# Kernel tuning notes

Hardware: AMD Instinct MI355X
Metric: run time of the kernel (lower is better)

## Reference

```python
import jax, jax.numpy as jnp
import numpy as np

B, C, H, W = 64, 512, 64, 64
RED = 16
HID = C // RED  # 32
N_EXPERTS = 3

def setup_inputs() -> dict:
    key = jax.random.key(0)
    k1, k2, k3, k4 = jax.random.split(key, 4)
    x = jax.random.normal(k1, (B, C, H, W), dtype=jnp.float32)
    dataset = jax.random.randint(k2, (B,), 0, N_EXPERTS, dtype=jnp.int32)
    # torch Linear weight layout: [out_features, in_features]
    W1 = jax.random.normal(k3, (N_EXPERTS, HID, C), dtype=jnp.float32) * (1.0 / np.sqrt(C))
    W2 = jax.random.normal(k4, (N_EXPERTS, C, HID), dtype=jnp.float32) * (1.0 / np.sqrt(HID))
    return {"x": x, "dataset": dataset, "W1": W1, "W2": W2}

def reference(x, dataset, W1, W2):
    # global average pool: [B, C]
    y = jnp.mean(x, axis=(2, 3))
    # per-sample expert weights, routed by dataset id
    w1 = W1[dataset]  # [B, HID, C]
    w2 = W2[dataset]  # [B, C, HID]
    h = jax.nn.relu(jnp.einsum('bc,bhc->bh', y, w1))
    gate = jax.nn.sigmoid(jnp.einsum('bh,bch->bc', h, w2))  # [B, C]
    return x * gate[:, :, None, None]
```

## Files before the change

### kernel.cpp

```cpp
#include <hip/hip_runtime.h>
#include <math.h>

#define NB 64
#define NC 512
#define NHW 4096
#define NHID 32

__global__ __launch_bounds__(256) void pool_kernel(const float* __restrict__ x,
                                                   float* __restrict__ y) {
    const int bc = blockIdx.x;
    const float4* __restrict__ xin =
        reinterpret_cast<const float4*>(x + (size_t)bc * NHW);
    const int tid = threadIdx.x;

    float s = 0.f;
#pragma unroll
    for (int i = 0; i < 4; ++i) {
        float4 v = xin[tid + i * 256];
        s += v.x + v.y + v.z + v.w;
    }
#pragma unroll
    for (int o = 32; o; o >>= 1) s += __shfl_down(s, o, 64);

    __shared__ float partial[4];
    const int wid = tid >> 6;
    if ((tid & 63) == 0) partial[wid] = s;
    __syncthreads();
    if (tid == 0) {
        float t = partial[0] + partial[1] + partial[2] + partial[3];
        y[bc] = t * (1.0f / NHW);
    }
}

__global__ __launch_bounds__(256) void gate_kernel(const float* __restrict__ y,
                                                   const int* __restrict__ dataset,
                                                   const float* __restrict__ W1,
                                                   const float* __restrict__ W2,
                                                   float* __restrict__ gate) {
    const int b = blockIdx.x;
    const int tid = threadIdx.x;

    __shared__ float ys[NC];
    __shared__ float hs[NHID];

    ys[tid]       = y[b * NC + tid];
    ys[tid + 256] = y[b * NC + tid + 256];
    const int e = dataset[b];
    __syncthreads();

    const int hid = tid >> 3;
    const int j   = tid & 7;
    const float* __restrict__ w1row = W1 + ((size_t)e * NHID + hid) * NC;
    float acc = 0.f;
    for (int c = j; c < NC; c += 8) acc += ys[c] * w1row[c];
#pragma unroll
    for (int o = 4; o; o >>= 1) acc += __shfl_down(acc, o, 8);
    if (j == 0) hs[hid] = fmaxf(acc, 0.f);
    __syncthreads();

    const float* __restrict__ w2base = W2 + (size_t)e * NC * NHID;
#pragma unroll
    for (int k = 0; k < 2; ++k) {
        const int c = tid + k * 256;
        const float* __restrict__ w2row = w2base + c * NHID;
        float z = 0.f;
#pragma unroll
        for (int hh = 0; hh < NHID; ++hh) z += hs[hh] * w2row[hh];
        gate[b * NC + c] = 1.0f / (1.0f + expf(-z));
    }
}

__global__ __launch_bounds__(256) void scale_kernel(const float* __restrict__ x,
                                                    const float* __restrict__ gate,
                                                    float* __restrict__ out) {
    const size_t total4 = (size_t)NB * NC * NHW / 4;
    const size_t stride = (size_t)gridDim.x * blockDim.x;
    for (size_t i = (size_t)blockIdx.x * 256 + threadIdx.x; i < total4; i += stride) {
        const float g = gate[i >> 10];
        float4 v = reinterpret_cast<const float4*>(x)[i];
        v.x *= g; v.y *= g; v.z *= g; v.w *= g;
        reinterpret_cast<float4*>(out)[i] = v;
    }
}

extern "C" void kernel_launch(void* const* d_in, const int* in_sizes, int n_in,
                              void* d_out, int out_size, void* d_ws, size_t ws_size,
                              hipStream_t stream) {
    const float* x       = (const float*)d_in[0];
    const int*   dataset = (const int*)d_in[1];
    const float* W1      = (const float*)d_in[2];
    const float* W2      = (const float*)d_in[3];
    float* out = (float*)d_out;

    float* y    = (float*)d_ws;
    float* gate = y + NB * NC;

    pool_kernel<<<NB * NC, 256, 0, stream>>>(x, y);
    gate_kernel<<<NB, 256, 0, stream>>>(y, dataset, W1, W2, gate);
    scale_kernel<<<2048, 256, 0, stream>>>(x, gate, out);
}
```

Baseline: 353.4 us.

## Use wave-per-plane pooling and reverse-order scale with nontemporal stores

```diff
diff --git a/kernel.cpp b/kernel.cpp
--- a/kernel.cpp
+++ b/kernel.cpp
@@ -5,31 +5,27 @@
 #define NC 512
 #define NHW 4096
 #define NHID 32
+#define NPLANES (NB * NC)
+
+typedef float f32x4 __attribute__((ext_vector_type(4)));
 
 __global__ __launch_bounds__(256) void pool_kernel(const float* __restrict__ x,
                                                    float* __restrict__ y) {
-    const int bc = blockIdx.x;
-    const float4* __restrict__ xin =
-        reinterpret_cast<const float4*>(x + (size_t)bc * NHW);
-    const int tid = threadIdx.x;
+    const int wid   = threadIdx.x >> 6;
+    const int lane  = threadIdx.x & 63;
+    const int plane = blockIdx.x * 4 + wid;
+    const f32x4* __restrict__ xin =
+        reinterpret_cast<const f32x4*>(x + (size_t)plane * NHW);
 
     float s = 0.f;
 #pragma unroll
-    for (int i = 0; i < 4; ++i) {
-        float4 v = xin[tid + i * 256];
+    for (int i = 0; i < 16; ++i) {
+        f32x4 v = xin[lane + i * 64];
         s += v.x + v.y + v.z + v.w;
     }
 #pragma unroll
     for (int o = 32; o; o >>= 1) s += __shfl_down(s, o, 64);
-
-    __shared__ float partial[4];
-    const int wid = tid >> 6;
-    if ((tid & 63) == 0) partial[wid] = s;
-    __syncthreads();
-    if (tid == 0) {
-        float t = partial[0] + partial[1] + partial[2] + partial[3];
-        y[bc] = t * (1.0f / NHW);
-    }
+    if (lane == 0) y[plane] = s * (1.0f / NHW);
 }
 
 __global__ __launch_bounds__(256) void gate_kernel(const float* __restrict__ y,
@@ -73,13 +69,28 @@
 __global__ __launch_bounds__(256) void scale_kernel(const float* __restrict__ x,
                                                     const float* __restrict__ gate,
                                                     float* __restrict__ out) {
-    const size_t total4 = (size_t)NB * NC * NHW / 4;
-    const size_t stride = (size_t)gridDim.x * blockDim.x;
-    for (size_t i = (size_t)blockIdx.x * 256 + threadIdx.x; i < total4; i += stride) {
-        const float g = gate[i >> 10];
-        float4 v = reinterpret_cast<const float4*>(x)[i];
-        v.x *= g; v.y *= g; v.z *= g; v.w *= g;
-        reinterpret_cast<float4*>(out)[i] = v;
+    const int pair = (NPLANES / 2 - 1) - blockIdx.x;
+    const int p0 = pair * 2;
+    const float g0 = gate[p0];
+    const float g1 = gate[p0 + 1];
+    const size_t base = (size_t)pair * 2048;
+    const f32x4* __restrict__ xin = reinterpret_cast<const f32x4*>(x);
+    f32x4* __restrict__ o4 = reinterpret_cast<f32x4*>(out);
+    const int t = threadIdx.x;
+
+#pragma unroll
+    for (int k = 0; k < 4; ++k) {
+        const size_t i = base + (size_t)k * 256 + t;
+        f32x4 v = xin[i];
+        v *= g0;
+        __builtin_nontemporal_store(v, &o4[i]);
+    }
+#pragma unroll
+    for (int k = 0; k < 4; ++k) {
+        const size_t i = base + 1024 + (size_t)k * 256 + t;
+        f32x4 v = xin[i];
+        v *= g1;
+        __builtin_nontemporal_store(v, &o4[i]);
     }
 }
 
@@ -95,7 +106,7 @@
     float* y    = (float*)d_ws;
     float* gate = y + NB * NC;
 
-    pool_kernel<<<NB * NC, 256, 0, stream>>>(x, y);
+    pool_kernel<<<NPLANES / 4, 256, 0, stream>>>(x, y);
     gate_kernel<<<NB, 256, 0, stream>>>(y, dataset, W1, W2, gate);
-    scale_kernel<<<2048, 256, 0, stream>>>(x, gate, out);
+    scale_kernel<<<NPLANES / 2, 256, 0, stream>>>(x, gate, out);
 }
```

Result: faster. 284.9 us (-19.4%).

## Fuse pool, gate and scale into one persistent kernel holding x in registers

Applied to the files above, without the earlier changes.

```diff
diff --git a/kernel.cpp b/kernel.cpp
--- a/kernel.cpp
+++ b/kernel.cpp
@@ -5,81 +5,139 @@
 #define NC 512
 #define NHW 4096
 #define NHID 32
+#define GRID 512
+#define BLK 256
+#define DSLOT 6
+#define OWNER_LAG 3
+#define CONS_LAG 6
 
-__global__ __launch_bounds__(256) void pool_kernel(const float* __restrict__ x,
-                                                   float* __restrict__ y) {
-    const int bc = blockIdx.x;
-    const float4* __restrict__ xin =
-        reinterpret_cast<const float4*>(x + (size_t)bc * NHW);
-    const int tid = threadIdx.x;
+typedef float f32x4 __attribute__((ext_vector_type(4)));
 
-    float s = 0.f;
+
+__global__ __launch_bounds__(BLK, 2) void fused_kernel(
+        const float* __restrict__ x,
+        const int* __restrict__ dataset,
+        const float* __restrict__ W1,
+        const float* __restrict__ W2,
+        float* __restrict__ out,
+        unsigned* __restrict__ done1,
+        unsigned* __restrict__ gready,
+        float* __restrict__ y,
+        float* __restrict__ gate) {
+    const int tid  = threadIdx.x;
+    const int blk  = blockIdx.x;
+    const int wid  = tid >> 6;
+    const int lane = tid & 63;
+    const int c0   = blk;
+    const int grp  = blk >> 3;
+
+    __shared__ float part[4];
+    __shared__ float ysl[NC];
+    __shared__ float hsl[NHID];
+    __shared__ float gbc;
+
+    const f32x4* __restrict__ x4 = reinterpret_cast<const f32x4*>(x);
+    f32x4* __restrict__ o4 = reinterpret_cast<f32x4*>(out);
+
+    f32x4 v[DSLOT][4];
+
+    for (int base = 0; base < NB + CONS_LAG + 2; base += DSLOT) {
 #pragma unroll
-    for (int i = 0; i < 4; ++i) {
-        float4 v = xin[tid + i * 256];
-        s += v.x + v.y + v.z + v.w;
-    }
+        for (int u = 0; u < DSLOT; ++u) {
+            const int t = base + u;
+
+            const int sc = t - CONS_LAG;
+            if (sc >= 0 && sc < NB) {
+                if (tid == 0) {
+                    while (__hip_atomic_load(&gready[sc], __ATOMIC_RELAXED,
+                                             __HIP_MEMORY_SCOPE_AGENT) == 0u) {
+                        __builtin_amdgcn_s_sleep(1);
+                    }
+                    gbc = __hip_atomic_load(&gate[sc * NC + c0], __ATOMIC_RELAXED,
+                                            __HIP_MEMORY_SCOPE_AGENT);
+                }
+                __syncthreads();
+                const float g = gbc;
+                const size_t pb = ((size_t)(sc * NC + c0) << 10) + tid;
 #pragma unroll
-    for (int o = 32; o; o >>= 1) s += __shfl_down(s, o, 64);
+                for (int k = 0; k < 4; ++k) {
+                    f32x4 w = v[u][k] * g;
+                    __builtin_nontemporal_store(w, &o4[pb + (size_t)(k << 8)]);
+                }
+            }
 
-    __shared__ float partial[4];
-    const int wid = tid >> 6;
-    if ((tid & 63) == 0) partial[wid] = s;
-    __syncthreads();
-    if (tid == 0) {
-        float t = partial[0] + partial[1] + partial[2] + partial[3];
-        y[bc] = t * (1.0f / NHW);
-    }
-}
+            const int sb = t - OWNER_LAG;
+            if (sb >= 0 && sb < NB && blk == sb * 8 + (sb & 7)) {
+                if (tid < 64) {
+                    for (;;) {
+                        unsigned cv = __hip_atomic_load(&done1[sb * 64 + tid],
+                                                        __ATOMIC_RELAXED,
+                                                        __HIP_MEMORY_SCOPE_AGENT);
+                        if (__all(cv == 8u)) break;
+                        __builtin_amdgcn_s_sleep(1);
+                    }
+                }
+                __syncthreads();
+                ysl[tid] = __hip_atomic_load(&y[sb * NC + tid], __ATOMIC_RELAXED,
+                                             __HIP_MEMORY_SCOPE_AGENT);
+                ysl[tid + 256] = __hip_atomic_load(&y[sb * NC + tid + 256],
+                                                   __ATOMIC_RELAXED,
+                                                   __HIP_MEMORY_SCOPE_AGENT);
+                const int e = dataset[sb];
+                __syncthreads();
+                {
+                    const int hid = tid >> 3, j = tid & 7;
+                    const float* __restrict__ w1row =
+                        W1 + ((size_t)e * NHID + hid) * NC;
+                    float acc = 0.f;
+                    for (int c = j; c < NC; c += 8) acc += ysl[c] * w1row[c];
+#pragma unroll
+                    for (int o = 4; o; o >>= 1) acc += __shfl_down(acc, o, 8);
+                    if (j == 0) hsl[hid] = fmaxf(acc, 0.f);
+                }
+                __syncthreads();
+                const float* __restrict__ w2base = W2 + (size_t)e * NC * NHID;
+#pragma unroll
+                for (int k = 0; k < 2; ++k) {
+                    const int c = tid + k * 256;
+                    const float* __restrict__ w2row = w2base + c * NHID;
+                    float z = 0.f;
+#pragma unroll
+                    for (int h = 0; h < NHID; ++h) z += hsl[h] * w2row[h];
+                    float gv = 1.0f / (1.0f + expf(-z));
+                    __hip_atomic_store(&gate[sb * NC + c], gv, __ATOMIC_RELAXED,
+                                       __HIP_MEMORY_SCOPE_AGENT);
+                }
+                __threadfence();
+                __syncthreads();
+                if (tid == 0)
+                    __hip_atomic_store(&gready[sb], 1u, __ATOMIC_RELEASE,
+                                       __HIP_MEMORY_SCOPE_AGENT);
+            }
 
-__global__ __launch_bounds__(256) void gate_kernel(const float* __restrict__ y,
-                                                   const int* __restrict__ dataset,
-                                                   const float* __restrict__ W1,
-                                                   const float* __restrict__ W2,
-                                                   float* __restrict__ gate) {
-    const int b = blockIdx.x;
-    const int tid = threadIdx.x;
+            if (t < NB) {
+                const size_t pb = ((size_t)(t * NC + c0) << 10) + tid;
+#pragma unroll
+                for (int k = 0; k < 4; ++k)
+                    v[u][k] = x4[pb + (size_t)(k << 8)];
 
-    __shared__ float ys[NC];
-    __shared__ float hs[NHID];
-
-    ys[tid]       = y[b * NC + tid];
-    ys[tid + 256] = y[b * NC + tid + 256];
-    const int e = dataset[b];
-    __syncthreads();
-
-    const int hid = tid >> 3;
-    const int j   = tid & 7;
-    const float* __restrict__ w1row = W1 + ((size_t)e * NHID + hid) * NC;
-    float acc = 0.f;
-    for (int c = j; c < NC; c += 8) acc += ys[c] * w1row[c];
+                f32x4 a = v[u][0] + v[u][1] + v[u][2] + v[u][3];
+                float s = a.x + a.y + a.z + a.w;
 #pragma unroll
-    for (int o = 4; o; o >>= 1) acc += __shfl_down(acc, o, 8);
-    if (j == 0) hs[hid] = fmaxf(acc, 0.f);
-    __syncthreads();
-
-    const float* __restrict__ w2base = W2 + (size_t)e * NC * NHID;
-#pragma unroll
-    for (int k = 0; k < 2; ++k) {
-        const int c = tid + k * 256;
-        const float* __restrict__ w2row = w2base + c * NHID;
-        float z = 0.f;
-#pragma unroll
-        for (int hh = 0; hh < NHID; ++hh) z += hs[hh] * w2row[hh];
-        gate[b * NC + c] = 1.0f / (1.0f + expf(-z));
-    }
-}
-
-__global__ __launch_bounds__(256) void scale_kernel(const float* __restrict__ x,
-                                                    const float* __restrict__ gate,
-                                                    float* __restrict__ out) {
-    const size_t total4 = (size_t)NB * NC * NHW / 4;
-    const size_t stride = (size_t)gridDim.x * blockDim.x;
-    for (size_t i = (size_t)blockIdx.x * 256 + threadIdx.x; i < total4; i += stride) {
-        const float g = gate[i >> 10];
-        float4 v = reinterpret_cast<const float4*>(x)[i];
-        v.x *= g; v.y *= g; v.z *= g; v.w *= g;
-        reinterpret_cast<float4*>(out)[i] = v;
+                for (int o = 32; o; o >>= 1) s += __shfl_down(s, o, 64);
+                __syncthreads();
+                if (lane == 0) part[wid] = s;
+                __syncthreads();
+                if (tid == 0) {
+                    float tot = part[0] + part[1] + part[2] + part[3];
+                    __hip_atomic_store(&y[t * NC + c0], tot * (1.0f / NHW),
+                                       __ATOMIC_RELAXED, __HIP_MEMORY_SCOPE_AGENT);
+                    __hip_atomic_fetch_add(&done1[t * 64 + grp], 1u,
+                                           __ATOMIC_RELEASE,
+                                           __HIP_MEMORY_SCOPE_AGENT);
+                }
+            }
+        }
     }
 }
 
@@ -92,10 +150,12 @@
     const float* W2      = (const float*)d_in[3];
     float* out = (float*)d_out;
 
-    float* y    = (float*)d_ws;
-    float* gate = y + NB * NC;
+    unsigned* done1  = (unsigned*)d_ws;
+    unsigned* gready = (unsigned*)((char*)d_ws + 16384);
+    float*    y      = (float*)((char*)d_ws + 32768);
+    float*    gate   = (float*)((char*)d_ws + 163840);
 
-    pool_kernel<<<NB * NC, 256, 0, stream>>>(x, y);
-    gate_kernel<<<NB, 256, 0, stream>>>(y, dataset, W1, W2, gate);
-    scale_kernel<<<2048, 256, 0, stream>>>(x, gate, out);
+    hipMemsetAsync(d_ws, 0, 32768, stream);
+    fused_kernel<<<GRID, BLK, 0, stream>>>(x, dataset, W1, W2, out,
+                                           done1, gready, y, gate);
 }
```

New measurement: 1.130 ms. 220% more time.
